# Optimization experiments

Measured on AMD Instinct MI355X. Metric: run time of the kernel, lower is better.

## Reference

```python
import jax, jax.numpy as jnp
import numpy as np

EPS = 0.05
H2 = 1e-4
ALPHA = 1.0 / EPS**2   # 400.0
BETA = 1.0 / H2        # 1e4


def setup_inputs() -> dict:
    key = jax.random.key(0)
    x0 = jax.random.normal(key, (16, 1, 1024, 1024), dtype=jnp.float32)
    return {"x0": x0}


def reference(x0) -> jnp.ndarray:
    # Replication pad by 1 on H and W (NCHW layout)
    up = jnp.pad(x0, ((0, 0), (0, 0), (1, 1), (1, 1)), mode="edge")
    # 5-point Laplacian stencil: N + S + W + E - 4*center (matches fixed 3x3 conv kernel)
    diffusion = (up[:, :, :-2, 1:-1] + up[:, :, 2:, 1:-1]
                 + up[:, :, 1:-1, :-2] + up[:, :, 1:-1, 2:]
                 - 4.0 * x0)
    # alpha*x - alpha*x^3 + beta*diffusion
    return ALPHA * x0 - ALPHA * x0**3 + BETA * diffusion
```

## Files before the change

### kernel.cpp

```cpp
#include <hip/hip_runtime.h>


#define ALPHA 400.0f
#define BETA  10000.0f

typedef float vfloat4 __attribute__((ext_vector_type(4)));

__global__ __launch_bounds__(256) void stencil_kernel(const float* __restrict__ x,
                                                      float* __restrict__ out) {
    constexpr int W = 1024;
    constexpr int H = 1024;
    constexpr int NUM_XCD = 8;

    const int band = gridDim.x / NUM_XCD;
    const int row  = (blockIdx.x & (NUM_XCD - 1)) * band + (blockIdx.x >> 3);

    const int x4 = threadIdx.x << 2;
    const int y  = row & (H - 1);
    const size_t img_off = (size_t)(row - y) * W;

    const float* img = x + img_off;

    const int yn = (y == 0)     ? 0     : y - 1;
    const int ys = (y == H - 1) ? H - 1 : y + 1;

    const vfloat4 c = *(const vfloat4*)(img + (size_t)y  * W + x4);
    const vfloat4 n = *(const vfloat4*)(img + (size_t)yn * W + x4);
    const vfloat4 s = *(const vfloat4*)(img + (size_t)ys * W + x4);

    const float wv = (x4 == 0)     ? c.x : img[(size_t)y * W + x4 - 1];
    const float ev = (x4 == W - 4) ? c.w : img[(size_t)y * W + x4 + 4];

    vfloat4 r;
    r.x = ALPHA * c.x - ALPHA * (c.x * c.x * c.x) + BETA * (n.x + s.x + wv  + c.y - 4.0f * c.x);
    r.y = ALPHA * c.y - ALPHA * (c.y * c.y * c.y) + BETA * (n.y + s.y + c.x + c.z - 4.0f * c.y);
    r.z = ALPHA * c.z - ALPHA * (c.z * c.z * c.z) + BETA * (n.z + s.z + c.y + c.w - 4.0f * c.z);
    r.w = ALPHA * c.w - ALPHA * (c.w * c.w * c.w) + BETA * (n.w + s.w + c.z + ev  - 4.0f * c.w);

    vfloat4* dst = (vfloat4*)(out + img_off + (size_t)y * W + x4);
    __builtin_nontemporal_store(r, dst);
}

extern "C" void kernel_launch(void* const* d_in, const int* in_sizes, int n_in,
                              void* d_out, int out_size, void* d_ws, size_t ws_size,
                              hipStream_t stream) {
    const float* x0 = (const float*)d_in[0];
    float* out = (float*)d_out;
    const int grid = out_size / 1024;
    stencil_kernel<<<grid, 256, 0, stream>>>(x0, out);
}
```

Baseline: 111.3 us.

## Process eight rows per block with register sliding window over rows

Each block now handles a strip of 8 consecutive rows instead of one. It keeps north, center and south rows in registers and slides them down, so each input row is loaded about once from global memory instead of three times. This cuts redundant L2 traffic and lowers block count by 8x. In exchange there is less parallelism (2048 blocks) and the loads inside the unrolled loop are serially dependent, which can reduce latency hiding.

```diff
diff --git a/kernel.cpp b/kernel.cpp
--- a/kernel.cpp
+++ b/kernel.cpp
@@ -10,35 +10,47 @@
                                                       float* __restrict__ out) {
     constexpr int W = 1024;
     constexpr int H = 1024;
+    constexpr int R = 8;
     constexpr int NUM_XCD = 8;
 
-    const int band = gridDim.x / NUM_XCD;
-    const int row  = (blockIdx.x & (NUM_XCD - 1)) * band + (blockIdx.x >> 3);
+    const int band  = gridDim.x / NUM_XCD;
+    const int strip = (blockIdx.x & (NUM_XCD - 1)) * band + (blockIdx.x >> 3);
 
-    const int x4 = threadIdx.x << 2;
-    const int y  = row & (H - 1);
-    const size_t img_off = (size_t)(row - y) * W;
+    const int row0 = strip * R;
+    const int y0   = row0 & (H - 1);
+    const int x4   = threadIdx.x << 2;
 
-    const float* img = x + img_off;
+    const size_t base = (size_t)row0 * W + x4;
+    const float* pc = x + base;
+    float*       po = out + base;
 
-    const int yn = (y == 0)     ? 0     : y - 1;
-    const int ys = (y == H - 1) ? H - 1 : y + 1;
+    const bool left  = (x4 == 0);
+    const bool right = (x4 == W - 4);
 
-    const vfloat4 c = *(const vfloat4*)(img + (size_t)y  * W + x4);
-    const vfloat4 n = *(const vfloat4*)(img + (size_t)yn * W + x4);
-    const vfloat4 s = *(const vfloat4*)(img + (size_t)ys * W + x4);
+    vfloat4 n = *(const vfloat4*)(pc - ((y0 == 0) ? 0 : W));
+    vfloat4 c = *(const vfloat4*)pc;
 
-    const float wv = (x4 == 0)     ? c.x : img[(size_t)y * W + x4 - 1];
-    const float ev = (x4 == W - 4) ? c.w : img[(size_t)y * W + x4 + 4];
+    #pragma unroll
+    for (int r = 0; r < R; ++r) {
+        const int y = y0 + r;
+        const vfloat4 s = *(const vfloat4*)(pc + ((y == H - 1) ? 0 : W));
 
-    vfloat4 r;
-    r.x = ALPHA * c.x - ALPHA * (c.x * c.x * c.x) + BETA * (n.x + s.x + wv  + c.y - 4.0f * c.x);
-    r.y = ALPHA * c.y - ALPHA * (c.y * c.y * c.y) + BETA * (n.y + s.y + c.x + c.z - 4.0f * c.y);
-    r.z = ALPHA * c.z - ALPHA * (c.z * c.z * c.z) + BETA * (n.z + s.z + c.y + c.w - 4.0f * c.z);
-    r.w = ALPHA * c.w - ALPHA * (c.w * c.w * c.w) + BETA * (n.w + s.w + c.z + ev  - 4.0f * c.w);
+        const float wv = left  ? c.x : pc[-1];
+        const float ev = right ? c.w : pc[4];
 
-    vfloat4* dst = (vfloat4*)(out + img_off + (size_t)y * W + x4);
-    __builtin_nontemporal_store(r, dst);
+        vfloat4 o;
+        o.x = ALPHA * c.x - ALPHA * (c.x * c.x * c.x) + BETA * (n.x + s.x + wv  + c.y - 4.0f * c.x);
+        o.y = ALPHA * c.y - ALPHA * (c.y * c.y * c.y) + BETA * (n.y + s.y + c.x + c.z - 4.0f * c.y);
+        o.z = ALPHA * c.z - ALPHA * (c.z * c.z * c.z) + BETA * (n.z + s.z + c.y + c.w - 4.0f * c.z);
+        o.w = ALPHA * c.w - ALPHA * (c.w * c.w * c.w) + BETA * (n.w + s.w + c.z + ev  - 4.0f * c.w);
+
+        __builtin_nontemporal_store(o, (vfloat4*)po);
+
+        n = c;
+        c = s;
+        pc += W;
+        po += W;
+    }
 }
 
 extern "C" void kernel_launch(void* const* d_in, const int* in_sizes, int n_in,
@@ -46,6 +58,8 @@
                               hipStream_t stream) {
     const float* x0 = (const float*)d_in[0];
     float* out = (float*)d_out;
-    const int grid = out_size / 1024;
+    constexpr int R = 8;
+    const int rows = out_size / 1024;
+    const int grid = rows / R;
     stencil_kernel<<<grid, 256, 0, stream>>>(x0, out);
 }
```

Result: no change. 112.0 us (+0.6%).
